# Optimization experiments

Measured on AMD Instinct MI355X. Metric: run time of the kernel, lower is better.

The kernel has to match this reference:

```python
import jax, jax.numpy as jnp
import numpy as np

EPS = 1e-5
K = 3

def _bn(x, g, b):
    # training-mode BatchNorm2d: batch stats over (N,H,W), biased variance
    m = jnp.mean(x, axis=(0, 2, 3), keepdims=True)
    v = jnp.var(x, axis=(0, 2, 3), keepdims=True)
    return (x - m) * jax.lax.rsqrt(v + EPS) * g[None, :, None, None] + b[None, :, None, None]

def _gelu(x):
    return jax.nn.gelu(x, approximate=False)

def _dyn_dw(x, aw1, ab1, aw2, ab2):
    # dynamic depthwise conv: per-sample k^2 softmax weights shared over channels
    b, c, h, w = x.shape
    gap = jnp.mean(x, axis=(2, 3))                              # (b,c)
    h1 = jax.nn.relu(jnp.einsum('oc,bc->bo', aw1, gap) + ab1)   # (b,c//8)
    kw = jax.nn.softmax(jnp.einsum('oc,bc->bo', aw2, h1) + ab2, axis=1)  # (b,k^2)
    xp = jnp.pad(x, ((0, 0), (0, 0), (1, 1), (1, 1)))
    out = jnp.zeros_like(x)
    idx = 0
    for i in range(K):
        for j in range(K):
            out = out + kw[:, idx, None, None, None] * xp[:, :, i:i + h, j:j + w]
            idx += 1
    return out

def _channel_att(x, w1, w2):
    avg = jnp.mean(x, axis=(2, 3))        # (b,C)
    mx = jnp.max(x, axis=(2, 3))          # (b,C)
    def fc(v):
        return jnp.einsum('oc,bc->bo', w2, jax.nn.relu(jnp.einsum('oc,bc->bo', w1, v)))
    s = jax.nn.sigmoid(fc(avg) + fc(mx))  # (b,C)
    return s[:, :, None, None] * x

def _forward(x, w1, b1, g1, be1, aw1, ab1, aw2, ab2, g2, be2,
             ca_w1, ca_w2, pw, pb, g3, be3, sw, sb):
    b, n, d = x.shape
    h = w = int(np.sqrt(n))
    residual = x
    xi = jnp.transpose(x.reshape(b, h, w, d), (0, 3, 1, 2))       # (b,d,h,w)
    # pw_expand: 1x1 conv -> GELU -> BN
    y = jnp.einsum('oc,bchw->bohw', w1, xi) + b1[None, :, None, None]
    y = _bn(_gelu(y), g1, be1)                                    # (b,4d,h,w)
    # dw_conv: dynamic depthwise -> GELU -> BN -> channel attention
    y = _dyn_dw(y, aw1, ab1, aw2, ab2)
    y = _bn(_gelu(y), g2, be2)
    y = _channel_att(y, ca_w1, ca_w2)
    # spatial attention
    avg_o = jnp.mean(y, axis=1, keepdims=True)
    max_o = jnp.max(y, axis=1, keepdims=True)
    sp_in = jnp.concatenate([avg_o, max_o], axis=1)               # (b,2,h,w)
    sp = jax.lax.conv_general_dilated(sp_in, sw, (1, 1), ((3, 3), (3, 3)),
                                      dimension_numbers=('NCHW', 'OIHW', 'NCHW'))
    sp = jax.nn.sigmoid(sp + sb[None, :, None, None])
    y = y * sp
    # pw_project: 1x1 conv -> BN
    y = jnp.einsum('oc,bchw->bohw', pw, y) + pb[None, :, None, None]
    y = _bn(y, g3, be3)
    y = jnp.transpose(y, (0, 2, 3, 1)).reshape(b, n, d)
    return residual + y

def setup_inputs() -> dict:
    key = jax.random.key(0)
    ks = jax.random.split(key, 16)
    d, C = 256, 1024
    def rn(k, shape, fan):
        return jax.random.normal(k, shape, jnp.float32) * np.float32(np.sqrt(2.0 / fan))
    return {
        'x': jax.random.normal(ks[0], (8, 1024, d), jnp.float32),
        'w1': rn(ks[1], (C, d), d), 'b1': jnp.zeros((C,), jnp.float32),
        'g1': jnp.ones((C,), jnp.float32), 'be1': jnp.zeros((C,), jnp.float32),
        'aw1': rn(ks[2], (C // 8, C), C), 'ab1': jnp.zeros((C // 8,), jnp.float32),
        'aw2': rn(ks[3], (K * K, C // 8), C // 8), 'ab2': jnp.zeros((K * K,), jnp.float32),
        'g2': jnp.ones((C,), jnp.float32), 'be2': jnp.zeros((C,), jnp.float32),
        'ca_w1': rn(ks[4], (C // 16, C), C), 'ca_w2': rn(ks[5], (C, C // 16), C // 16),
        'pw': rn(ks[6], (d, C), C), 'pb': jnp.zeros((d,), jnp.float32),
        'g3': jnp.ones((d,), jnp.float32), 'be3': jnp.zeros((d,), jnp.float32),
        'sw': rn(ks[7], (1, 2, 7, 7), 2 * 49), 'sb': jnp.zeros((1,), jnp.float32),
    }

def reference(x, w1, b1, g1, be1, aw1, ab1, aw2, ab2, g2, be2,
              ca_w1, ca_w2, pw, pb, g3, be3, sw, sb):
    return _forward(x, w1, b1, g1, be1, aw1, ab1, aw2, ab2, g2, be2,
                    ca_w1, ca_w2, pw, pb, g3, be3, sw, sb)
```

## Files before the change

### kernel.cpp

```cpp
#include <hip/hip_runtime.h>
#include <math.h>

constexpr int B = 8;
constexpr int D = 256;
constexpr int C = 1024;
constexpr int H = 32, W = 32;
constexpr int P = H * W;
constexpr int M = B * P;
constexpr float EPS = 1e-5f;

typedef unsigned short u16;
typedef unsigned int u32;
typedef __attribute__((ext_vector_type(8))) short short8;
typedef __attribute__((ext_vector_type(4))) float floatx4;

constexpr size_t WS_CHSUM1 = 0;
constexpr size_t WS_CHSQ1  = 1024;
constexpr size_t WS_GAPSUM = 2048;
constexpr size_t WS_CHSUM3 = 10240;
constexpr size_t WS_CHSQ3  = 10496;
constexpr size_t WS_CHSUM2 = 10752;
constexpr size_t WS_CHSQ2  = 11776;
constexpr size_t WS_BSUM2  = 12800;
constexpr size_t WS_UMAX2  = 20992;
constexpr size_t WS_UMAXN2 = 29184;
constexpr size_t WS_ACC_COUNT = 37376;
constexpr size_t WS_SCALE1 = 37376;
constexpr size_t WS_SHIFT1 = 38400;
constexpr size_t WS_KW     = 39424;
constexpr size_t WS_SCALE2 = 39680;
constexpr size_t WS_SHIFT2 = 40704;
constexpr size_t WS_SATT   = 41728;
constexpr size_t WS_AVGO   = 49920;
constexpr size_t WS_MAXO   = 58112;
constexpr size_t WS_SP     = 66304;
constexpr size_t WS_PRE    = 74496;
constexpr size_t WS_T1B    = 2171648;
constexpr size_t WS_T2B    = 6365952;
constexpr size_t WS_XB     = 10560256;
constexpr size_t WS_W1B    = 11608832;
constexpr size_t WS_PWB    = 11739904;
constexpr size_t WS_PWBF   = 11870976;
constexpr size_t WS_BIAS2  = 12919552;

__device__ __forceinline__ float gelu_exact(float v) {
    return 0.5f * v * (1.0f + erff(v * 0.70710678118654752440f));
}

__device__ __forceinline__ u16 f2bf(float f) {
    u32 u = __float_as_uint(f);
    u += 0x7fff + ((u >> 16) & 1);
    return (u16)(u >> 16);
}

__device__ __forceinline__ float bf2f(u16 v) {
    return __uint_as_float(((u32)v) << 16);
}

__device__ __forceinline__ u32 fkey(float f) {
    u32 u = __float_as_uint(f);
    return (u & 0x80000000u) ? ~u : (u | 0x80000000u);
}
__device__ __forceinline__ float fkeyinv(u32 k) {
    return __uint_as_float((k & 0x80000000u) ? (k ^ 0x80000000u) : ~k);
}

#define GLOAD(SRC, DST) __builtin_amdgcn_global_load_lds( \
    (const __attribute__((address_space(1))) void*)(SRC), \
    (__attribute__((address_space(3))) void*)(DST), 16, 0, 0)

__global__ __launch_bounds__(256) void cvt_all_kernel(const float* __restrict__ x,
                                                      const float* __restrict__ w1,
                                                      u16* __restrict__ xb,
                                                      u16* __restrict__ w1b,
                                                      float* __restrict__ acc_zero) {
    const int i = blockIdx.x * 256 + threadIdx.x;
    if (i < (int)WS_ACC_COUNT) acc_zero[i] = 0.f;
    const float* src;
    u16* dst;
    int off;
    if (i < 524288) { src = x;  dst = xb;  off = i; }
    else            { src = w1; dst = w1b; off = i - 524288; }
    const float4 v = *(const float4*)(src + (size_t)off * 4);
    uint2 o;
    o.x = ((u32)f2bf(v.x)) | ((u32)f2bf(v.y) << 16);
    o.y = ((u32)f2bf(v.z)) | ((u32)f2bf(v.w) << 16);
    *(uint2*)(dst + (size_t)off * 4) = o;
}

template<int KD, int EPI, int NS, int MB, int NB, int WSPLIT>
__global__ __launch_bounds__(256 * WSPLIT) void mfma_gemm_kernel(
    const u16* __restrict__ A,
    const u16* __restrict__ Bw,
    const float* __restrict__ bias,
    const float* __restrict__ bias_post,
    const float* __restrict__ avg_o,
    const float* __restrict__ max_o,
    const float* __restrict__ swp,
    const float* __restrict__ sbp,
    void* __restrict__ outv,
    float* __restrict__ csum,
    float* __restrict__ csq,
    float* __restrict__ gsum)
{
    constexpr int NT = 256 * WSPLIT;
    constexpr int MI = MB / 32;
    constexpr int NJ = NB / 32;
    constexpr int ABUF = MB * 32;
    constexpr int BBUF = NB * 32;
    constexpr int BUFSZ = ABUF + BBUF;
    constexpr int GA = MB / 64;
    constexpr int GB = NB / 64;
    constexpr int LD = GA + GB;
    static_assert(LD == 3, "vmcnt literals assume 3 loads per chunk");
    constexpr int NCH = KD / 32;
    constexpr int NCHG = NCH / WSPLIT;
    constexpr int GX = NS / NB;
    constexpr int NWG = (M / MB) * GX;
    constexpr int CPX = NWG / 8;
    extern __shared__ u16 smem[];
    const int t = threadIdx.x;
    const int lane = t & 63;
    const int wv = t >> 6;
    const int grp = (WSPLIT == 2) ? (wv >> 2) : 0;
    const int wg = wv & 3;
    const int tg = t & 255;

    const int lin = blockIdx.y * GX + blockIdx.x;
    const int swz = (lin & 7) * CPX + (lin >> 3);
    const int bx = swz % GX;
    const int by = swz / GX;
    const int row0 = by * MB;
    const int col0 = bx * NB;
    const int bb = row0 >> 10;

    const int wrow = (wg >> 1) * (MB / 2);
    const int wcol = (wg & 1) * (NB / 2);
    const int lm = lane & 15;
    const int lk8 = (lane >> 4) * 8;
    const int srow = tg >> 2;
    const int scol = (tg & 3) * 8;
    const u16* gA = A + (size_t)(row0 + srow) * KD + scol;
    const u16* gB = Bw + (EPI == 1 ? (size_t)bb * NS * KD : (size_t)0)
                       + (size_t)(col0 + srow) * KD + scol;
    const float* biasp = bias + (EPI == 1 ? bb * NS : 0);

    u16* gsmem = smem + grp * (3 * BUFSZ);
    const int kbase = grp * NCHG;

    const floatx4 zero = {0.f, 0.f, 0.f, 0.f};
    floatx4 acc[MI][NJ];
#pragma unroll
    for (int i = 0; i < MI; ++i)
#pragma unroll
        for (int j = 0; j < NJ; ++j) acc[i][j] = zero;

    auto stage = [&](u16* buf, int c) {
        const int kk = (kbase + c) * 32;
        u16* As = buf;
        u16* Bs = buf + ABUF;
#pragma unroll
        for (int g = 0; g < GA; ++g)
            GLOAD(gA + (size_t)g * 64 * KD + kk, As + g * 2048 + tg * 8);
#pragma unroll
        for (int g = 0; g < GB; ++g)
            GLOAD(gB + (size_t)g * 64 * KD + kk, Bs + g * 2048 + tg * 8);
    };
    auto compute = [&](const u16* buf) {
        const u16* As = buf;
        const u16* Bs = buf + ABUF;
        short8 af[MI], bf[NJ];
#pragma unroll
        for (int i = 0; i < MI; ++i)
            af[i] = *(const short8*)(As + (wrow + i * 16 + lm) * 32 + lk8);
#pragma unroll
        for (int j = 0; j < NJ; ++j)
            bf[j] = *(const short8*)(Bs + (wcol + j * 16 + lm) * 32 + lk8);
#pragma unroll
        for (int i = 0; i < MI; ++i)
#pragma unroll
            for (int j = 0; j < NJ; ++j)
                acc[i][j] = __builtin_amdgcn_mfma_f32_16x16x32_bf16(af[i], bf[j], acc[i][j], 0, 0, 0);
    };

    stage(gsmem, 0);
    if (NCHG > 1) stage(gsmem + BUFSZ, 1);

    float* ext = (float*)(smem + (size_t)WSPLIT * 3 * BUFSZ);
    if constexpr (EPI == 1) {
        const int p0 = (by & 7) * MB;
        const int h0 = p0 >> 5;
        const int bbase = bb * P;
        for (int e = t; e < 640; e += NT) {
            const bool isM = e >= 320;
            const int idx = isM ? e - 320 : e;
            const int r = idx >> 5, w = idx & 31;
            const int hh = h0 - 3 + r;
            float v = 0.f;
            if (hh >= 0 && hh < H) v = (isM ? max_o : avg_o)[bbase + hh * W + w];
            ext[e] = v;
        }
        if (t < 98) ext[640 + t] = swp[t];
        __syncthreads();
        if (t < 128) {
            const int hl = t >> 5, w = t & 31;
            float a = sbp[0];
#pragma unroll
            for (int i = 0; i < 7; ++i) {
                const int r = hl + i;
#pragma unroll
                for (int j = 0; j < 7; ++j) {
                    const int ww = w + j - 3;
                    if (ww < 0 || ww >= W) continue;
                    a = fmaf(ext[640 + i * 7 + j], ext[r * 32 + ww], a);
                    a = fmaf(ext[640 + 49 + i * 7 + j], ext[320 + r * 32 + ww], a);
                }
            }
            ext[768 + t] = 1.0f / (1.0f + expf(-a));
        }
    }

    int cur = 0;
    for (int c = 0; c < NCHG; ++c) {
        if (c + 2 < NCHG) {
            const int nb3 = (cur + 2 >= 3) ? cur - 1 : cur + 2;
            stage(gsmem + nb3 * BUFSZ, c + 2);
            asm volatile("s_waitcnt vmcnt(6)" ::: "memory");
        } else if (c + 1 < NCHG) {
            asm volatile("s_waitcnt vmcnt(3)" ::: "memory");
        } else {
            asm volatile("s_waitcnt vmcnt(0)" ::: "memory");
        }
        __builtin_amdgcn_s_barrier();
        compute(gsmem + cur * BUFSZ);
        asm volatile("s_waitcnt lgkmcnt(0)" ::: "memory");
        __builtin_amdgcn_s_barrier();
        cur = (cur + 1 >= 3) ? 0 : cur + 1;
    }

    if constexpr (WSPLIT == 2) {
        float* red = (float*)(smem + 3 * BUFSZ);
        if (grp == 1) {
#pragma unroll
            for (int i = 0; i < MI; ++i)
#pragma unroll
                for (int r = 0; r < 4; ++r) {
                    const int lrow = wrow + i * 16 + (lane >> 4) * 4 + r;
#pragma unroll
                    for (int j = 0; j < NJ; ++j)
                        red[lrow * NB + wcol + j * 16 + lm] = acc[i][j][r];
                }
        }
        __syncthreads();
        if (grp == 0) {
#pragma unroll
            for (int i = 0; i < MI; ++i)
#pragma unroll
                for (int r = 0; r < 4; ++r) {
                    const int lrow = wrow + i * 16 + (lane >> 4) * 4 + r;
#pragma unroll
                    for (int j = 0; j < NJ; ++j)
                        acc[i][j][r] += red[lrow * NB + wcol + j * 16 + lm];
                }
        }
        __syncthreads();
    }

    float colsum[NJ], colsq[NJ];
#pragma unroll
    for (int j = 0; j < NJ; ++j) { colsum[j] = 0.f; colsq[j] = 0.f; }

    if (EPI == 0) {
        u16* Cs = smem;
#pragma unroll
        for (int i = 0; i < MI; ++i) {
#pragma unroll
            for (int r = 0; r < 4; ++r) {
                const int lrow = wrow + i * 16 + (lane >> 4) * 4 + r;
#pragma unroll
                for (int j = 0; j < NJ; ++j) {
                    const int lcol = wcol + j * 16 + lm;
                    const float tv = gelu_exact(acc[i][j][r] + biasp[col0 + lcol]);
                    Cs[lrow * NB + lcol] = f2bf(tv);
                    colsum[j] += tv;
                    colsq[j] = fmaf(tv, tv, colsq[j]);
                }
            }
        }
        __syncthreads();
        constexpr int TPR = NB / 8;
        constexpr int RPP = NT / TPR;
        u16* outp = (u16*)outv;
#pragma unroll
        for (int pp = 0; pp < MB / RPP; ++pp) {
            const int r = pp * RPP + t / TPR;
            const int cc = (t % TPR) * 8;
            *(uint4*)(outp + (size_t)(row0 + r) * NS + col0 + cc) =
                *(const uint4*)(Cs + r * NB + cc);
        }
    } else {
        float* Cs = (float*)smem;
        if (grp == 0) {
#pragma unroll
            for (int i = 0; i < MI; ++i) {
#pragma unroll
                for (int r = 0; r < 4; ++r) {
                    const int lrow = wrow + i * 16 + (lane >> 4) * 4 + r;
                    const float rs = ext[768 + lrow];
#pragma unroll
                    for (int j = 0; j < NJ; ++j) {
                        const int lcol = wcol + j * 16 + lm;
                        const float tv = rs * (acc[i][j][r] + biasp[col0 + lcol])
                                       + bias_post[col0 + lcol];
                        Cs[lrow * NB + lcol] = tv;
                        colsum[j] += tv;
                        colsq[j] = fmaf(tv, tv, colsq[j]);
                    }
                }
            }
        }
        __syncthreads();
        constexpr int TPR = NB / 4;
        constexpr int RPP = NT / TPR;
        float* outp = (float*)outv;
#pragma unroll
        for (int pp = 0; pp < MB / RPP; ++pp) {
            const int r = pp * RPP + t / TPR;
            const int cc = (t % TPR) * 4;
            *(float4*)(outp + (size_t)(row0 + r) * NS + col0 + cc) =
                *(const float4*)(Cs + r * NB + cc);
        }
    }

#pragma unroll
    for (int j = 0; j < NJ; ++j) {
        float s = colsum[j];
        float q = colsq[j];
        s += __shfl_xor(s, 16); s += __shfl_xor(s, 32);
        q += __shfl_xor(q, 16); q += __shfl_xor(q, 32);
        if (grp == 0 && lane < 16) {
            const int c = col0 + wcol + j * 16 + lm;
            atomicAdd(&csum[c], s);
            atomicAdd(&csq[c], q);
            if (EPI == 0) atomicAdd(&gsum[bb * NS + c], s);
        }
    }
}

__global__ __launch_bounds__(1024) void dynmlp_kernel(const float* __restrict__ chsum1,
                                                      const float* __restrict__ chsq1,
                                                      const float* __restrict__ gapsum,
                                                      const float* __restrict__ g1,
                                                      const float* __restrict__ be1,
                                                      const float* __restrict__ aw1,
                                                      const float* __restrict__ ab1,
                                                      const float* __restrict__ aw2,
                                                      const float* __restrict__ ab2,
                                                      float* __restrict__ scale1,
                                                      float* __restrict__ shift1,
                                                      float* __restrict__ kw) {
    const int b = blockIdx.x;
    const int t = threadIdx.x;
    const int wave = t >> 6, lane = t & 63;
    __shared__ float g[1024];
    __shared__ float h1[128];
    __shared__ float logits[12];
    {
        const float m = chsum1[t] * (1.0f / (float)M);
        const float var = chsq1[t] * (1.0f / (float)M) - m * m;
        const float rstd = rsqrtf(var + EPS);
        const float sc = rstd * g1[t];
        const float sh = be1[t] - m * sc;
        if (b == 0) { scale1[t] = sc; shift1[t] = sh; }
        g[t] = gapsum[b * C + t] * (1.0f / (float)P) * sc + sh;
    }
    __syncthreads();
#pragma unroll
    for (int k = 0; k < 8; ++k) {
        const int u = wave * 8 + k;
        const float4* wr = (const float4*)(aw1 + (size_t)u * C);
        float s = 0.f;
#pragma unroll
        for (int ch = 0; ch < 4; ++ch) {
            const float4 wv = wr[lane + 64 * ch];
            const float4 sv = *(const float4*)(g + 4 * lane + 256 * ch);
            s += wv.x * sv.x + wv.y * sv.y + wv.z * sv.z + wv.w * sv.w;
        }
#pragma unroll
        for (int off = 1; off < 64; off <<= 1) s += __shfl_xor(s, off);
        if (lane == 0) h1[u] = fmaxf(s + ab1[u], 0.f);
    }
    __syncthreads();
    if (wave < 9) {
        float s = aw2[wave * 128 + lane] * h1[lane]
                + aw2[wave * 128 + 64 + lane] * h1[64 + lane];
#pragma unroll
        for (int off = 1; off < 64; off <<= 1) s += __shfl_xor(s, off);
        if (lane == 0) logits[wave] = s + ab2[wave];
    }
    __syncthreads();
    if (t == 0) {
        float mx = logits[0];
        for (int i = 1; i < 9; ++i) mx = fmaxf(mx, logits[i]);
        float e[9], den = 0.f;
        for (int i = 0; i < 9; ++i) { e[i] = expf(logits[i] - mx); den += e[i]; }
        const float inv = 1.0f / den;
        for (int i = 0; i < 9; ++i) kw[b * 9 + i] = e[i] * inv;
    }
}

__global__ __launch_bounds__(256) void dwconv_kernel(const u16* __restrict__ t1b,
                                                     const float* __restrict__ scale1,
                                                     const float* __restrict__ shift1,
                                                     const float* __restrict__ kw,
                                                     u16* __restrict__ t2b,
                                                     float* __restrict__ chsum2,
                                                     float* __restrict__ chsq2,
                                                     float* __restrict__ bsum2,
                                                     u32* __restrict__ umax2,
                                                     u32* __restrict__ umaxn2) {
    __shared__ u16 rows[3 * 32 * 256];
    const int lin = blockIdx.y * 4 + blockIdx.x;
    const int xcd = lin & 7;
    const int i7 = lin >> 3;
    const int b = i7 >> 4;
    const int r4 = i7 & 15;
    const int h = xcd * 4 + (r4 >> 2);
    const int cq = r4 & 3;
    const int t = threadIdx.x;

    const u16* gbase = t1b + (size_t)b * P * C + cq * 256;
#pragma unroll
    for (int i = 0; i < 12; ++i) {
        const int lin2 = i * 256 + t;
        const int chunk = lin2 >> 5;
        const int r = chunk >> 5;
        const int w = chunk & 31;
        const int off8 = (lin2 & 31) * 8;
        const int hr = h + r - 1;
        uint4 v = {0u, 0u, 0u, 0u};
        if (hr >= 0 && hr < H)
            v = *(const uint4*)(gbase + (size_t)(hr * W + w) * C + off8);
        *(uint4*)(&rows[chunk * 256 + off8]) = v;
    }
    __syncthreads();

    const int c = t;
    const int gc = cq * 256 + c;
    float kk[9];
#pragma unroll
    for (int i = 0; i < 9; ++i) kk[i] = kw[b * 9 + i];
    const float sc = scale1[gc];
    const float sh = shift1[gc];
    float scm[3], shm[3];
    scm[0] = (h > 0)     ? sc : 0.f;  shm[0] = (h > 0)     ? sh : 0.f;
    scm[1] = sc;                      shm[1] = sh;
    scm[2] = (h < H - 1) ? sc : 0.f;  shm[2] = (h < H - 1) ? sh : 0.f;

    const u16* rp0 = rows + c;
#define DWVAL(ri, w) fmaf(bf2f(rp0[((ri) * 32 + (w)) * 256]), scm[ri], shm[ri])

    float vm0 = 0.f, vm1 = 0.f, vm2 = 0.f;
    float vc0 = DWVAL(0, 0), vc1 = DWVAL(1, 0), vc2 = DWVAL(2, 0);
    float vp0 = DWVAL(0, 1), vp1 = DWVAL(1, 1), vp2 = DWVAL(2, 1);

    float s = 0.f, q = 0.f, mx = -INFINITY, mn = INFINITY;
    u16* orow = t2b + ((size_t)b * P + h * W) * C + gc;
    for (int w = 0; w < W; ++w) {
        float acc;
        acc = kk[0] * vm0;
        acc = fmaf(kk[1], vc0, acc);
        acc = fmaf(kk[2], vp0, acc);
        acc = fmaf(kk[3], vm1, acc);
        acc = fmaf(kk[4], vc1, acc);
        acc = fmaf(kk[5], vp1, acc);
        acc = fmaf(kk[6], vm2, acc);
        acc = fmaf(kk[7], vc2, acc);
        acc = fmaf(kk[8], vp2, acc);
        const float y = gelu_exact(acc);
        orow[(size_t)w * C] = f2bf(y);
        s += y;
        q = fmaf(y, y, q);
        mx = fmaxf(mx, y);
        mn = fminf(mn, y);
        vm0 = vc0; vc0 = vp0;
        vm1 = vc1; vc1 = vp1;
        vm2 = vc2; vc2 = vp2;
        if (w + 2 < W) {
            vp0 = DWVAL(0, w + 2);
            vp1 = DWVAL(1, w + 2);
            vp2 = DWVAL(2, w + 2);
        } else {
            vp0 = 0.f; vp1 = 0.f; vp2 = 0.f;
        }
    }
#undef DWVAL
    atomicAdd(&chsum2[gc], s);
    atomicAdd(&chsq2[gc], q);
    atomicAdd(&bsum2[b * C + gc], s);
    atomicMax(&umax2[b * C + gc], fkey(mx));
    atomicMax(&umaxn2[b * C + gc], fkey(-mn));
}

__global__ __launch_bounds__(1024) void chatt_kernel(const float* __restrict__ chsum2,
                                                     const float* __restrict__ chsq2,
                                                     const float* __restrict__ bsum2,
                                                     const u32* __restrict__ umax2,
                                                     const u32* __restrict__ umaxn2,
                                                     const float* __restrict__ g2,
                                                     const float* __restrict__ be2,
                                                     const float* __restrict__ caw1,
                                                     const float* __restrict__ caw2,
                                                     float* __restrict__ scale2,
                                                     float* __restrict__ shift2,
                                                     float* __restrict__ s_att) {
    const int b = blockIdx.x;
    const int t = threadIdx.x;
    const int wave = t >> 6, lane = t & 63;
    __shared__ float la[1024], lx[1024], ha[64], hm[64];
    {
        const float m = chsum2[t] * (1.0f / (float)M);
        const float var = chsq2[t] * (1.0f / (float)M) - m * m;
        const float rstd = rsqrtf(var + EPS);
        const float sc = rstd * g2[t];
        const float sh = be2[t] - m * sc;
        if (b == 0) { scale2[t] = sc; shift2[t] = sh; }
        la[t] = bsum2[b * C + t] * (1.0f / (float)P) * sc + sh;
        const float mx = fkeyinv(umax2[b * C + t]);
        const float mn = -fkeyinv(umaxn2[b * C + t]);
        lx[t] = (sc >= 0.f ? mx : mn) * sc + sh;
    }
    __syncthreads();
#pragma unroll
    for (int k = 0; k < 8; ++k) {
        const int u = wave * 8 + k;
        const int row = u & 63;
        const float* src = (u < 64) ? la : lx;
        const float4* wr = (const float4*)(caw1 + (size_t)row * C);
        float s = 0.f;
#pragma unroll
        for (int ch = 0; ch < 4; ++ch) {
            const float4 wv = wr[lane + 64 * ch];
            const float4 sv = *(const float4*)(src + 4 * lane + 256 * ch);
            s += wv.x * sv.x + wv.y * sv.y + wv.z * sv.z + wv.w * sv.w;
        }
#pragma unroll
        for (int off = 1; off < 64; off <<= 1) s += __shfl_xor(s, off);
        if (lane == 0) {
            s = fmaxf(s, 0.f);
            if (u < 64) ha[row] = s; else hm[row] = s;
        }
    }
    __syncthreads();
    {
        const float4* w2 = (const float4*)(caw2 + (size_t)t * 64);
        float s = 0.f;
#pragma unroll
        for (int j = 0; j < 16; ++j) {
            const float4 wv = w2[j];
            s += wv.x * (ha[j * 4 + 0] + hm[j * 4 + 0]);
            s += wv.y * (ha[j * 4 + 1] + hm[j * 4 + 1]);
            s += wv.z * (ha[j * 4 + 2] + hm[j * 4 + 2]);
            s += wv.w * (ha[j * 4 + 3] + hm[j * 4 + 3]);
        }
        s_att[b * C + t] = 1.0f / (1.0f + expf(-s));
    }
}

__global__ __launch_bounds__(256) void yqfold_kernel(const u16* __restrict__ t2b,
                                                     const float* __restrict__ scale2,
                                                     const float* __restrict__ shift2,
                                                     const float* __restrict__ s_att,
                                                     const float* __restrict__ pw,
                                                     float* __restrict__ avg_o,
                                                     float* __restrict__ max_o,
                                                     u16* __restrict__ pwb,
                                                     float* __restrict__ bias2) {
    const int bid = blockIdx.x;
    const int t = threadIdx.x;
    const int wave = t >> 6, lane = t & 63;
    __shared__ float r0[4], r1[4];
    if (bid < M) {
        const int row = bid;
        const int b = row >> 10;
        const int c0 = t * 4;
        const uint2 vv = *(const uint2*)(t2b + (size_t)row * C + c0);
        const float v0 = bf2f((u16)(vv.x & 0xffff));
        const float v1 = bf2f((u16)(vv.x >> 16));
        const float v2 = bf2f((u16)(vv.y & 0xffff));
        const float v3 = bf2f((u16)(vv.y >> 16));
        const float4 sc = *(const float4*)(scale2 + c0);
        const float4 sh = *(const float4*)(shift2 + c0);
        const float4 sa = *(const float4*)(s_att + (size_t)b * C + c0);
        const float y0 = fmaf(v0, sc.x, sh.x) * sa.x;
        const float y1 = fmaf(v1, sc.y, sh.y) * sa.y;
        const float y2 = fmaf(v2, sc.z, sh.z) * sa.z;
        const float y3 = fmaf(v3, sc.w, sh.w) * sa.w;
        float s = (y0 + y1) + (y2 + y3);
        float mx = fmaxf(fmaxf(y0, y1), fmaxf(y2, y3));
#pragma unroll
        for (int off = 32; off > 0; off >>= 1) {
            s += __shfl_down(s, off);
            mx = fmaxf(mx, __shfl_down(mx, off));
        }
        if (lane == 0) { r0[wave] = s; r1[wave] = mx; }
        __syncthreads();
        if (t == 0) {
            const float S = r0[0] + r0[1] + r0[2] + r0[3];
            const float Mx = fmaxf(fmaxf(r1[0], r1[1]), fmaxf(r1[2], r1[3]));
            avg_o[row] = S * (1.0f / (float)C);
            max_o[row] = Mx;
        }
    } else {
        const int bd = bid - M;
        const int b = bd >> 8;
        const int d = bd & 255;
        const int c0 = t * 4;
        const float4 wv = *(const float4*)(pw + (size_t)d * C + c0);
        const float4 sc = *(const float4*)(scale2 + c0);
        const float4 sh = *(const float4*)(shift2 + c0);
        const float4 sa = *(const float4*)(s_att + (size_t)b * C + c0);
        uint2 o;
        o.x = ((u32)f2bf(wv.x * sc.x * sa.x)) | ((u32)f2bf(wv.y * sc.y * sa.y) << 16);
        o.y = ((u32)f2bf(wv.z * sc.z * sa.z)) | ((u32)f2bf(wv.w * sc.w * sa.w) << 16);
        *(uint2*)(pwb + ((size_t)b * D + d) * C + c0) = o;
        float s = wv.x * sh.x * sa.x + wv.y * sh.y * sa.y
                + wv.z * sh.z * sa.z + wv.w * sh.w * sa.w;
#pragma unroll
        for (int off = 1; off < 64; off <<= 1) s += __shfl_xor(s, off);
        if (lane == 0) r0[wave] = s;
        __syncthreads();
        if (t == 0) bias2[bd] = r0[0] + r0[1] + r0[2] + r0[3];
    }
}

__global__ __launch_bounds__(256) void final_kernel(const float* __restrict__ x,
                                                    const float* __restrict__ pre,
                                                    const float* __restrict__ chsum3,
                                                    const float* __restrict__ chsq3,
                                                    const float* __restrict__ g3,
                                                    const float* __restrict__ be3,
                                                    float* __restrict__ out) {
    __shared__ float lsc[256], lsh[256];
    const int t = threadIdx.x;
    {
        const float m = chsum3[t] * (1.0f / (float)M);
        const float var = chsq3[t] * (1.0f / (float)M) - m * m;
        const float rstd = rsqrtf(var + EPS);
        const float sc = rstd * g3[t];
        lsc[t] = sc;
        lsh[t] = be3[t] - m * sc;
    }
    __syncthreads();
    const int i = blockIdx.x * 256 + t;
    const int e = i * 4;
    const int d = e & 255;
    const float4 xv = *(const float4*)(x + e);
    const float4 pv = *(const float4*)(pre + e);
    const float4 sc = *(const float4*)(lsc + d);
    const float4 sh = *(const float4*)(lsh + d);
    float4 o;
    o.x = xv.x + fmaf(pv.x, sc.x, sh.x);
    o.y = xv.y + fmaf(pv.y, sc.y, sh.y);
    o.z = xv.z + fmaf(pv.z, sc.z, sh.z);
    o.w = xv.w + fmaf(pv.w, sc.w, sh.w);
    *(float4*)(out + e) = o;
}

extern "C" void kernel_launch(void* const* d_in, const int* in_sizes, int n_in,
                              void* d_out, int out_size, void* d_ws, size_t ws_size,
                              hipStream_t stream) {
    const float* x    = (const float*)d_in[0];
    const float* w1   = (const float*)d_in[1];
    const float* b1   = (const float*)d_in[2];
    const float* g1   = (const float*)d_in[3];
    const float* be1  = (const float*)d_in[4];
    const float* aw1  = (const float*)d_in[5];
    const float* ab1  = (const float*)d_in[6];
    const float* aw2  = (const float*)d_in[7];
    const float* ab2  = (const float*)d_in[8];
    const float* g2   = (const float*)d_in[9];
    const float* be2  = (const float*)d_in[10];
    const float* caw1 = (const float*)d_in[11];
    const float* caw2 = (const float*)d_in[12];
    const float* pw   = (const float*)d_in[13];
    const float* pb   = (const float*)d_in[14];
    const float* g3   = (const float*)d_in[15];
    const float* be3  = (const float*)d_in[16];
    const float* sw   = (const float*)d_in[17];
    const float* sb   = (const float*)d_in[18];
    float* out = (float*)d_out;
    float* ws = (float*)d_ws;

    float* chsum1  = ws + WS_CHSUM1;
    float* chsq1   = ws + WS_CHSQ1;
    float* gapsum  = ws + WS_GAPSUM;
    float* chsum3  = ws + WS_CHSUM3;
    float* chsq3   = ws + WS_CHSQ3;
    float* chsum2  = ws + WS_CHSUM2;
    float* chsq2   = ws + WS_CHSQ2;
    float* bsum2   = ws + WS_BSUM2;
    u32*   umax2   = (u32*)(ws + WS_UMAX2);
    u32*   umaxn2  = (u32*)(ws + WS_UMAXN2);
    float* scale1  = ws + WS_SCALE1;
    float* shift1  = ws + WS_SHIFT1;
    float* kw      = ws + WS_KW;
    float* scale2  = ws + WS_SCALE2;
    float* shift2  = ws + WS_SHIFT2;
    float* s_att   = ws + WS_SATT;
    float* avg_o   = ws + WS_AVGO;
    float* max_o   = ws + WS_MAXO;
    float* pre     = ws + WS_PRE;
    float* bias2   = ws + WS_BIAS2;
    u16* t1b  = (u16*)(ws + WS_T1B);
    u16* t2b  = (u16*)(ws + WS_T2B);
    u16* xb   = (u16*)(ws + WS_XB);
    u16* w1b  = (u16*)(ws + WS_W1B);
    u16* pwbf = (u16*)(ws + WS_PWBF);

    cvt_all_kernel<<<dim3(2304), 256, 0, stream>>>(x, w1, xb, w1b, ws);
    mfma_gemm_kernel<256, 0, C, 128, 64, 1><<<dim3(C / 64, M / 128), 256, 36864, stream>>>(
        xb, w1b, b1, nullptr, nullptr, nullptr, nullptr, nullptr,
        t1b, chsum1, chsq1, gapsum);
    dynmlp_kernel<<<dim3(B), 1024, 0, stream>>>(chsum1, chsq1, gapsum, g1, be1,
                                                aw1, ab1, aw2, ab2, scale1, shift1, kw);
    dwconv_kernel<<<dim3(4, B * H), 256, 0, stream>>>(t1b, scale1, shift1, kw, t2b,
                                                      chsum2, chsq2, bsum2, umax2, umaxn2);
    chatt_kernel<<<dim3(B), 1024, 0, stream>>>(chsum2, chsq2, bsum2, umax2, umaxn2,
                                               g2, be2, caw1, caw2, scale2, shift2, s_att);
    yqfold_kernel<<<dim3(M + B * D), 256, 0, stream>>>(t2b, scale2, shift2, s_att, pw,
                                                       avg_o, max_o, pwbf, bias2);
    mfma_gemm_kernel<1024, 1, D, 128, 64, 2><<<dim3(D / 64, M / 128), 512, 77312, stream>>>(
        t2b, pwbf, bias2, pb, avg_o, max_o, sw, sb,
        pre, chsum3, chsq3, nullptr);
    final_kernel<<<dim3((M * D / 4) / 256), 256, 0, stream>>>(x, pre, chsum3, chsq3, g3, be3, out);
}
```

Before: 197.6 us.

## Map one row per wave in yqfold and raise MFMA wave priority

The yqfold kernel now assigns each 1024-element row (and each folded pw row) to a single wave, with 16 elements per lane. This removes the shared-memory reduction and __syncthreads, cuts the block count by four, and allows wider 128-bit loads and stores. Separately, the GEMM compute lambda raises wave priority with s_setprio around the MFMA loop to favour the math instructions over other waves. The risk is that fewer, heavier blocks could lower latency hiding, and the priority change may have little effect.

```diff
diff --git a/kernel.cpp b/kernel.cpp
--- a/kernel.cpp
+++ b/kernel.cpp
@@ -176,11 +176,13 @@
 #pragma unroll
         for (int j = 0; j < NJ; ++j)
             bf[j] = *(const short8*)(Bs + (wcol + j * 16 + lm) * 32 + lk8);
+        __builtin_amdgcn_s_setprio(1);
 #pragma unroll
         for (int i = 0; i < MI; ++i)
 #pragma unroll
             for (int j = 0; j < NJ; ++j)
                 acc[i][j] = __builtin_amdgcn_mfma_f32_16x16x32_bf16(af[i], bf[j], acc[i][j], 0, 0, 0);
+        __builtin_amdgcn_s_setprio(0);
     };
 
     stage(gsmem, 0);
@@ -579,58 +581,64 @@
     const int bid = blockIdx.x;
     const int t = threadIdx.x;
     const int wave = t >> 6, lane = t & 63;
-    __shared__ float r0[4], r1[4];
-    if (bid < M) {
-        const int row = bid;
+    const int c0 = lane * 16;
+    const float4* scp = (const float4*)(scale2 + c0);
+    const float4* shp = (const float4*)(shift2 + c0);
+    if (bid < M / 4) {
+        const int row = bid * 4 + wave;
         const int b = row >> 10;
-        const int c0 = t * 4;
-        const uint2 vv = *(const uint2*)(t2b + (size_t)row * C + c0);
-        const float v0 = bf2f((u16)(vv.x & 0xffff));
-        const float v1 = bf2f((u16)(vv.x >> 16));
-        const float v2 = bf2f((u16)(vv.y & 0xffff));
-        const float v3 = bf2f((u16)(vv.y >> 16));
-        const float4 sc = *(const float4*)(scale2 + c0);
-        const float4 sh = *(const float4*)(shift2 + c0);
-        const float4 sa = *(const float4*)(s_att + (size_t)b * C + c0);
-        const float y0 = fmaf(v0, sc.x, sh.x) * sa.x;
-        const float y1 = fmaf(v1, sc.y, sh.y) * sa.y;
-        const float y2 = fmaf(v2, sc.z, sh.z) * sa.z;
-        const float y3 = fmaf(v3, sc.w, sh.w) * sa.w;
-        float s = (y0 + y1) + (y2 + y3);
-        float mx = fmaxf(fmaxf(y0, y1), fmaxf(y2, y3));
-#pragma unroll
-        for (int off = 32; off > 0; off >>= 1) {
-            s += __shfl_down(s, off);
-            mx = fmaxf(mx, __shfl_down(mx, off));
-        }
-        if (lane == 0) { r0[wave] = s; r1[wave] = mx; }
-        __syncthreads();
-        if (t == 0) {
-            const float S = r0[0] + r0[1] + r0[2] + r0[3];
-            const float Mx = fmaxf(fmaxf(r1[0], r1[1]), fmaxf(r1[2], r1[3]));
-            avg_o[row] = S * (1.0f / (float)C);
-            max_o[row] = Mx;
+        const u16* tr = t2b + (size_t)row * C + c0;
+        const uint4 va = *(const uint4*)tr;
+        const uint4 vb = *(const uint4*)(tr + 8);
+        const float4* sap = (const float4*)(s_att + (size_t)b * C + c0);
+        const u32 words[8] = {va.x, va.y, va.z, va.w, vb.x, vb.y, vb.z, vb.w};
+        float s = 0.f, mx = -INFINITY;
+#pragma unroll
+        for (int q = 0; q < 4; ++q) {
+            const float4 sc4 = scp[q], sh4 = shp[q], sa4 = sap[q];
+            const u32 lo = words[2 * q], hi = words[2 * q + 1];
+            const float y0 = fmaf(bf2f((u16)(lo & 0xffff)), sc4.x, sh4.x) * sa4.x;
+            const float y1 = fmaf(bf2f((u16)(lo >> 16)),    sc4.y, sh4.y) * sa4.y;
+            const float y2 = fmaf(bf2f((u16)(hi & 0xffff)), sc4.z, sh4.z) * sa4.z;
+            const float y3 = fmaf(bf2f((u16)(hi >> 16)),    sc4.w, sh4.w) * sa4.w;
+            s += (y0 + y1) + (y2 + y3);
+            mx = fmaxf(mx, fmaxf(fmaxf(y0, y1), fmaxf(y2, y3)));
+        }
+#pragma unroll
+        for (int off = 1; off < 64; off <<= 1) {
+            s += __shfl_xor(s, off);
+            mx = fmaxf(mx, __shfl_xor(mx, off));
+        }
+        if (lane == 0) {
+            avg_o[row] = s * (1.0f / (float)C);
+            max_o[row] = mx;
         }
     } else {
-        const int bd = bid - M;
+        const int bd = (bid - M / 4) * 4 + wave;
         const int b = bd >> 8;
         const int d = bd & 255;
-        const int c0 = t * 4;
-        const float4 wv = *(const float4*)(pw + (size_t)d * C + c0);
-        const float4 sc = *(const float4*)(scale2 + c0);
-        const float4 sh = *(const float4*)(shift2 + c0);
-        const float4 sa = *(const float4*)(s_att + (size_t)b * C + c0);
-        uint2 o;
-        o.x = ((u32)f2bf(wv.x * sc.x * sa.x)) | ((u32)f2bf(wv.y * sc.y * sa.y) << 16);
-        o.y = ((u32)f2bf(wv.z * sc.z * sa.z)) | ((u32)f2bf(wv.w * sc.w * sa.w) << 16);
-        *(uint2*)(pwb + ((size_t)b * D + d) * C + c0) = o;
-        float s = wv.x * sh.x * sa.x + wv.y * sh.y * sa.y
-                + wv.z * sh.z * sa.z + wv.w * sh.w * sa.w;
+        const float4* pwp = (const float4*)(pw + (size_t)d * C + c0);
+        const float4* sap = (const float4*)(s_att + (size_t)b * C + c0);
+        u32 o[8];
+        float s = 0.f;
+#pragma unroll
+        for (int q = 0; q < 4; ++q) {
+            const float4 w4 = pwp[q], sc4 = scp[q], sh4 = shp[q], sa4 = sap[q];
+            const float f0 = w4.x * sc4.x * sa4.x;
+            const float f1 = w4.y * sc4.y * sa4.y;
+            const float f2 = w4.z * sc4.z * sa4.z;
+            const float f3 = w4.w * sc4.w * sa4.w;
+            o[2 * q]     = ((u32)f2bf(f0)) | ((u32)f2bf(f1) << 16);
+            o[2 * q + 1] = ((u32)f2bf(f2)) | ((u32)f2bf(f3) << 16);
+            s += w4.x * sh4.x * sa4.x + w4.y * sh4.y * sa4.y
+               + w4.z * sh4.z * sa4.z + w4.w * sh4.w * sa4.w;
+        }
+        u16* pwbr = pwb + ((size_t)b * D + d) * C + c0;
+        *(uint4*)pwbr = *(uint4*)&o[0];
+        *(uint4*)(pwbr + 8) = *(uint4*)&o[4];
 #pragma unroll
         for (int off = 1; off < 64; off <<= 1) s += __shfl_xor(s, off);
-        if (lane == 0) r0[wave] = s;
-        __syncthreads();
-        if (t == 0) bias2[bd] = r0[0] + r0[1] + r0[2] + r0[3];
+        if (lane == 0) bias2[bd] = s;
     }
 }
 
@@ -728,8 +736,8 @@
                                                       chsum2, chsq2, bsum2, umax2, umaxn2);
     chatt_kernel<<<dim3(B), 1024, 0, stream>>>(chsum2, chsq2, bsum2, umax2, umaxn2,
                                                g2, be2, caw1, caw2, scale2, shift2, s_att);
-    yqfold_kernel<<<dim3(M + B * D), 256, 0, stream>>>(t2b, scale2, shift2, s_att, pw,
-                                                       avg_o, max_o, pwbf, bias2);
+    yqfold_kernel<<<dim3(M / 4 + (B * D) / 4), 256, 0, stream>>>(
+        t2b, scale2, shift2, s_att, pw, avg_o, max_o, pwbf, bias2);
     mfma_gemm_kernel<1024, 1, D, 128, 64, 2><<<dim3(D / 64, M / 128), 512, 77312, stream>>>(
         t2b, pwbf, bias2, pb, avg_o, max_o, sw, sb,
         pre, chsum3, chsq3, nullptr);
```

New measurement: 200.1 us. No clear change (+1.2%).
